# Performance work log

Hardware: AMD Instinct MI355X
Metric: run time of the kernel (lower is better)

Reference implementation:

```python
import jax, jax.numpy as jnp
import numpy as np

N, E, D, H = 20000, 320000, 128, 256
NUM_FINE = 2


def _mlp(x, W1, b1, W2, b2):
    # Linear -> relu -> Linear -> relu (dropout rate 0.0 is identity)
    h = jax.nn.relu(x @ W1 + b1)
    return jax.nn.relu(h @ W2 + b2)


def setup_inputs() -> dict:
    key = jax.random.key(0)
    ks = jax.random.split(key, 12)

    def p(k, shape):
        fan_in = shape[0]
        return jax.random.normal(k, shape, jnp.float32) * (1.0 / fan_in) ** 0.5

    return {
        "nodes": jax.random.normal(ks[0], (N, D), jnp.float32),
        "edges": jax.random.normal(ks[1], (E, D), jnp.float32),
        "senders": jax.random.randint(ks[2], (E,), 0, N, jnp.int32),
        "receivers": jax.random.randint(ks[3], (E,), 0, N, jnp.int32),
        # embed node MLP: D -> H -> D
        "Wn1": p(ks[4], (D, H)), "bn1": jnp.zeros((H,), jnp.float32),
        "Wn2": p(ks[5], (H, D)), "bn2": jnp.zeros((D,), jnp.float32),
        # embed edge MLP: D -> H -> D
        "We1": p(ks[6], (D, H)), "be1": jnp.zeros((H,), jnp.float32),
        "We2": p(ks[7], (H, D)), "be2": jnp.zeros((D,), jnp.float32),
        # edge model MLP: 3D -> H -> D  (concat[src, dest, edge_attr])
        "Wed1": p(ks[8], (3 * D, H)), "bed1": jnp.zeros((H,), jnp.float32),
        "Wed2": p(ks[9], (H, D)), "bed2": jnp.zeros((D,), jnp.float32),
        # node model MLP: 2D -> H -> D  (concat[x, segment_sum(edge_attr)])
        "Wnd1": p(ks[10], (2 * D, H)), "bnd1": jnp.zeros((H,), jnp.float32),
        "Wnd2": p(ks[11], (H, D)), "bnd2": jnp.zeros((D,), jnp.float32),
    }


def reference(nodes, edges, senders, receivers,
              Wn1, bn1, Wn2, bn2, We1, be1, We2, be2,
              Wed1, bed1, Wed2, bed2, Wnd1, bnd1, Wnd2, bnd2):
    # Embed stage (EmbedMetaLayer)
    x = _mlp(nodes, Wn1, bn1, Wn2, bn2)   # (N, D)
    e = _mlp(edges, We1, be1, We2, be2)   # (E, D)

    pooled = []
    for _ in range(NUM_FINE):
        # EdgeModel: gather src/dest node feats, concat with edge feats, MLP
        edge_in = jnp.concatenate([x[senders], x[receivers], e], axis=-1)  # (E, 3D)
        e = _mlp(edge_in, Wed1, bed1, Wed2, bed2)                           # (E, D)
        # NodeModel: scatter-add edge feats to receiver nodes, concat, MLP
        agg = jax.ops.segment_sum(e, receivers, num_segments=N)            # (N, D)
        x = _mlp(jnp.concatenate([x, agg], axis=-1), Wnd1, bnd1, Wnd2, bnd2)  # (N, D)
        # global_add_pooling: vmap(jnp.sum) over nodes -> per-node feature sum (N,)
        pooled.append(jnp.sum(x, axis=-1))
    # concatenate along last axis of the 1-D pooled vectors -> (NUM_FINE * N,)
    return jnp.concatenate(pooled, axis=-1)
```

## Files before the change

### kernel.cpp

```cpp
#include <hip/hip_runtime.h>
#include <stdint.h>

#define N_NODES 20000
#define N_EDGES 320000

typedef __attribute__((ext_vector_type(8)))  __bf16        bf16x8;
typedef __attribute__((ext_vector_type(16))) float         f32x16;
typedef __attribute__((ext_vector_type(4)))  float         f32x4v;
typedef __attribute__((ext_vector_type(4)))  uint32_t      u32x4;
typedef __attribute__((ext_vector_type(8)))  unsigned short us8;
typedef __attribute__((ext_vector_type(2)))  unsigned short us2;

static __device__ __forceinline__ unsigned short cvt_bf16(float f) {
  uint32_t u = __builtin_bit_cast(uint32_t, f);
  u = (u + 0x7fffu + ((u >> 16) & 1u)) >> 16;
  return (unsigned short)u;
}
static __device__ __forceinline__ float cvt_f32(unsigned short h) {
  uint32_t u = ((uint32_t)h) << 16;
  return __builtin_bit_cast(float, u);
}

static __device__ __forceinline__ void gll16(const void* g, void* l) {
  __builtin_amdgcn_global_load_lds(
      (const __attribute__((address_space(1))) unsigned int*)g,
      (__attribute__((address_space(3))) unsigned int*)l, 16, 0, 0);
}

__global__ void pack_w(const float* __restrict__ W, unsigned short* __restrict__ out,
                       int K, int Ncols) {
  int idx = blockIdx.x * 256 + threadIdx.x;
  int total = K * Ncols;
  if (idx >= total) return;
  int e    = idx & 7;
  int lane = (idx >> 3) & 63;
  int t    = idx >> 9;
  int ntiles = Ncols >> 5;
  int nt = t % ntiles;
  int ks = t / ntiles;
  int k = ks * 16 + (lane >> 5) * 8 + e;
  int c = nt * 32 + (lane & 31);
  out[idx] = cvt_bf16(W[(size_t)k * Ncols + c]);
}

__global__ void pack_w2(const float* __restrict__ W, unsigned short* __restrict__ out) {
  int idx = blockIdx.x * 256 + threadIdx.x;
  if (idx >= 32768) return;
  int e    = idx & 7;
  int lane = (idx >> 3) & 63;
  int t    = idx >> 9;
  int nt = t & 3, ks = t >> 2;
  int k = ks * 16 + ((lane >> 5) << 2) + (e & 3) + ((e >> 2) << 3);
  int c = nt * 32 + (lane & 31);
  out[idx] = cvt_bf16(W[(size_t)k * 128 + c]);
}

__global__ void hist_k(const int* __restrict__ recv, int* __restrict__ cnt, int n) {
  int i = blockIdx.x * 256 + threadIdx.x;
  if (i < n) atomicAdd(&cnt[recv[i]], 1);
}

__global__ void scan_k(const int* __restrict__ cnt, int* __restrict__ off,
                       int* __restrict__ cursor, int n) {
  __shared__ int part[1024];
  int t = threadIdx.x;
  int chunk = (n + 1023) / 1024;
  int base = t * chunk;
  int s = 0;
  for (int i = 0; i < chunk; ++i) { int idx = base + i; if (idx < n) s += cnt[idx]; }
  part[t] = s;
  __syncthreads();
  for (int d = 1; d < 1024; d <<= 1) {
    int v = (t >= d) ? part[t - d] : 0;
    __syncthreads();
    part[t] += v;
    __syncthreads();
  }
  int prefix = (t > 0) ? part[t - 1] : 0;
  for (int i = 0; i < chunk; ++i) {
    int idx = base + i;
    if (idx < n) { off[idx] = prefix; cursor[idx] = prefix; prefix += cnt[idx]; }
  }
  if (t == 1023) off[n] = part[1023];
}

__global__ void fill_k(const int* __restrict__ recv, int* __restrict__ cursor,
                       int* __restrict__ eid, int n) {
  int i = blockIdx.x * 256 + threadIdx.x;
  if (i < n) {
    int p = atomicAdd(&cursor[recv[i]], 1);
    eid[p] = i;
  }
}

__global__ void agg_k(const unsigned short* __restrict__ eb, const int* __restrict__ off,
                      const int* __restrict__ eid, unsigned short* __restrict__ aggb, int n) {
  int node = blockIdx.x * 4 + (threadIdx.x >> 6);
  if (node >= n) return;
  int lane = threadIdx.x & 63;
  float a0 = 0.f, a1 = 0.f;
  int s = off[node], t = off[node + 1];
  for (int q = s; q < t; ++q) {
    int ei = eid[q];
    us2 v = *(const us2*)(eb + (size_t)ei * 128 + lane * 2);
    a0 += cvt_f32(v[0]);
    a1 += cvt_f32(v[1]);
  }
  us2 r; r[0] = cvt_bf16(a0); r[1] = cvt_bf16(a1);
  *(us2*)(aggb + (size_t)node * 128 + lane * 2) = r;
}

template <int KIN, int MODE, int POOL>
__global__ __launch_bounds__(256, 2)
void mlp_kernel(const float* __restrict__ srcf,
                const unsigned short* __restrict__ xb,
                const unsigned short* __restrict__ ebuf,
                const unsigned short* __restrict__ aggb,
                const int* __restrict__ senders,
                const int* __restrict__ receivers,
                const unsigned short* __restrict__ P1,
                const float* __restrict__ b1,
                const unsigned short* __restrict__ P2,
                const float* __restrict__ b2,
                unsigned short* __restrict__ dst,
                float* __restrict__ pool_out,
                int nrows) {
  constexpr int NS1 = KIN / 32;
  __shared__ __align__(16) unsigned char lds[32768];

  const int tid  = threadIdx.x;
  const int lane = tid & 63;
  const int wid  = tid >> 6;
  const int g    = lane >> 5;
  const int l31  = lane & 31;
  const int rowBlock = blockIdx.x << 7;

  const unsigned char* P1b = (const unsigned char*)P1;
  const unsigned char* P2b = (const unsigned char*)P2;

  int grow = rowBlock + wid * 32 + l31;
  if (grow >= nrows) grow = nrows - 1;

  const unsigned short *pS = nullptr, *pR = nullptr, *pE = nullptr;
  const unsigned short *pX = nullptr, *pAg = nullptr;
  const float* fb = nullptr;
  if constexpr (MODE == 0) {
    fb = srcf + (size_t)grow * KIN;
  } else if constexpr (MODE == 1) {
    pS = xb + (size_t)senders[grow] * 128;
    pR = xb + (size_t)receivers[grow] * 128;
    pE = ebuf + (size_t)grow * 128;
  } else {
    pX  = xb + (size_t)grow * 128;
    pAg = aggb + (size_t)grow * 128;
  }

  auto STG1 = [&](int s) {
    unsigned char* bW = lds + (s & 1) * 16384;
#pragma unroll
    for (int c = 0; c < 4; ++c)
      gll16(P1b + (size_t)s * 16384 + c * 4096 + tid * 16,
            bW + c * 4096 + wid * 1024);
  };
  auto STG2 = [&](int c) {
    unsigned char* bW = lds + (c & 1) * 16384;
#pragma unroll
    for (int q = 0; q < 4; ++q)
      gll16(P2b + (size_t)c * 16384 + q * 4096 + tid * 16,
            bW + q * 4096 + wid * 1024);
  };

  auto LROW = [&](int s, us8& o0, us8& o1) {
    const int k0s = s * 32;
    const unsigned short* p;
    if constexpr (MODE == 1) {
      const int seg = k0s >> 7;
      p = (seg == 0) ? pS : (seg == 1) ? pR : pE;
    } else {
      p = (k0s >> 7) ? pAg : pX;
    }
    const int ko = k0s & 127;
    o0 = *(const us8*)(p + ko + g * 8);
    o1 = *(const us8*)(p + ko + 16 + g * 8);
  };
  auto LROWF = [&](int s, f32x4v* rf) {
    const float* p = fb + s * 32 + g * 8;
    rf[0] = *(const f32x4v*)(p);
    rf[1] = *(const f32x4v*)(p + 4);
    rf[2] = *(const f32x4v*)(p + 16);
    rf[3] = *(const f32x4v*)(p + 20);
  };
  auto MKBR = [&](const f32x4v* rf, bf16x8& b0v, bf16x8& b1v) {
    us8 h0, h1;
#pragma unroll
    for (int e = 0; e < 4; ++e) {
      h0[e] = cvt_bf16(rf[0][e]); h0[4 + e] = cvt_bf16(rf[1][e]);
      h1[e] = cvt_bf16(rf[2][e]); h1[4 + e] = cvt_bf16(rf[3][e]);
    }
    b0v = __builtin_bit_cast(bf16x8, h0);
    b1v = __builtin_bit_cast(bf16x8, h1);
  };

  f32x16 acc1[8];
#pragma unroll
  for (int t = 0; t < 8; ++t)
#pragma unroll
    for (int k = 0; k < 16; ++k) acc1[t][k] = 0.0f;

  auto COMPUTE = [&](const unsigned char* bW, bf16x8 b0v, bf16x8 b1v) {
    __builtin_amdgcn_s_setprio(1);
#pragma unroll
    for (int kc = 0; kc < 2; ++kc) {
      const bf16x8 bv = kc ? b1v : b0v;
#pragma unroll
      for (int nt = 0; nt < 8; ++nt) {
        bf16x8 av = __builtin_bit_cast(bf16x8,
            *(const us8*)(bW + (kc * 8 + nt) * 1024 + lane * 16));
        acc1[nt] = __builtin_amdgcn_mfma_f32_32x32x16_bf16(av, bv, acc1[nt], 0, 0, 0);
      }
    }
    __builtin_amdgcn_s_setprio(0);
  };

  constexpr int CNT = (MODE == 0) ? 8 : 6;

  us8 rA0, rA1, rB0, rB1;
  f32x4v rfA[4], rfB[4];

  STG1(0);
  if constexpr (MODE == 0) LROWF(0, rfA); else LROW(0, rA0, rA1);

#pragma unroll 1
  for (int s = 0; s < NS1; s += 2) {
    STG1(s + 1);
    if constexpr (MODE == 0) LROWF(s + 1, rfB); else LROW(s + 1, rB0, rB1);
    asm volatile("s_waitcnt vmcnt(%0)" :: "i"(CNT) : "memory");
    asm volatile("s_barrier" ::: "memory");
    {
      bf16x8 b0v, b1v;
      if constexpr (MODE == 0) MKBR(rfA, b0v, b1v);
      else { b0v = __builtin_bit_cast(bf16x8, rA0); b1v = __builtin_bit_cast(bf16x8, rA1); }
      COMPUTE(lds, b0v, b1v);
    }
    asm volatile("s_waitcnt lgkmcnt(0)" ::: "memory");
    asm volatile("s_barrier" ::: "memory");

    const bool more = (s + 2 < NS1);
    if (more) {
      STG1(s + 2);
      if constexpr (MODE == 0) LROWF(s + 2, rfA); else LROW(s + 2, rA0, rA1);
      asm volatile("s_waitcnt vmcnt(%0)" :: "i"(CNT) : "memory");
    } else {
      asm volatile("s_waitcnt vmcnt(0)" ::: "memory");
    }
    asm volatile("s_barrier" ::: "memory");
    {
      bf16x8 b0v, b1v;
      if constexpr (MODE == 0) MKBR(rfB, b0v, b1v);
      else { b0v = __builtin_bit_cast(bf16x8, rB0); b1v = __builtin_bit_cast(bf16x8, rB1); }
      COMPUTE(lds + 16384, b0v, b1v);
    }
    if (more) {
      asm volatile("s_waitcnt lgkmcnt(0)" ::: "memory");
      asm volatile("s_barrier" ::: "memory");
    }
  }

  f32x4v bb[8];
#pragma unroll
  for (int t = 0; t < 8; ++t)
    bb[t] = *(const f32x4v*)(b1 + t * 32 + (lane & 7) * 4);

  STG2(0);
  asm volatile("s_waitcnt lgkmcnt(0)" ::: "memory");
  asm volatile("s_barrier" ::: "memory");
  STG2(1);

  u32x4 pa4[16];
#pragma unroll
  for (int t = 0; t < 8; ++t) {
#pragma unroll
    for (int q4 = 0; q4 < 4; ++q4) {
      const f32x4v bv4 = *(const f32x4v*)(b1 + t * 32 + q4 * 8 + g * 4);
      float v0 = fmaxf(acc1[t][q4 * 4 + 0] + bv4[0], 0.0f);
      float v1 = fmaxf(acc1[t][q4 * 4 + 1] + bv4[1], 0.0f);
      float v2 = fmaxf(acc1[t][q4 * 4 + 2] + bv4[2], 0.0f);
      float v3 = fmaxf(acc1[t][q4 * 4 + 3] + bv4[3], 0.0f);
      uint32_t lo, hi;
      asm("v_cvt_pk_bf16_f32 %0, %1, %2" : "=v"(lo) : "v"(v0), "v"(v1));
      asm("v_cvt_pk_bf16_f32 %0, %1, %2" : "=v"(hi) : "v"(v2), "v"(v3));
      pa4[t * 2 + (q4 >> 1)][(q4 & 1) * 2 + 0] = lo;
      pa4[t * 2 + (q4 >> 1)][(q4 & 1) * 2 + 1] = hi;
    }
  }

  f32x16 acc2[4];
#pragma unroll
  for (int nt = 0; nt < 4; ++nt)
#pragma unroll
    for (int k = 0; k < 16; ++k) acc2[nt][k] = 0.0f;

#pragma unroll
  for (int c = 0; c < 4; ++c) {
    if (c < 3) asm volatile("s_waitcnt vmcnt(4)" ::: "memory");
    else       asm volatile("s_waitcnt vmcnt(0)" ::: "memory");
    asm volatile("s_barrier" ::: "memory");
    const unsigned char* bW = lds + (c & 1) * 16384;
    __builtin_amdgcn_s_setprio(1);
#pragma unroll
    for (int kk = 0; kk < 4; ++kk) {
      const bf16x8 a2 = __builtin_bit_cast(bf16x8, pa4[c * 4 + kk]);
#pragma unroll
      for (int nt = 0; nt < 4; ++nt) {
        const bf16x8 bw = __builtin_bit_cast(bf16x8,
            *(const us8*)(bW + (kk * 4 + nt) * 1024 + lane * 16));
        acc2[nt] = __builtin_amdgcn_mfma_f32_32x32x16_bf16(a2, bw, acc2[nt], 0, 0, 0);
      }
    }
    __builtin_amdgcn_s_setprio(0);
    asm volatile("s_waitcnt lgkmcnt(0)" ::: "memory");
    asm volatile("s_barrier" ::: "memory");
    if (c + 2 < 4) STG2(c + 2);
  }

  float bias2[4];
#pragma unroll
  for (int nt = 0; nt < 4; ++nt) bias2[nt] = b2[nt * 32 + l31];

#pragma unroll
  for (int reg = 0; reg < 16; ++reg) {
    const int rowpat = (reg & 3) + ((reg >> 2) << 3) + g * 4;
    const int row = rowBlock + wid * 32 + rowpat;
    float vs = 0.0f;
#pragma unroll
    for (int nt = 0; nt < 4; ++nt) {
      float v = fmaxf(acc2[nt][reg] + bias2[nt], 0.0f);
      vs += v;
      if (row < nrows) dst[(size_t)row * 128 + nt * 32 + l31] = cvt_bf16(v);
    }
    if constexpr (POOL) {
#pragma unroll
      for (int m = 1; m <= 16; m <<= 1) vs += __shfl_xor(vs, m, 64);
      if (l31 == 0 && row < nrows) pool_out[row] = vs;
    }
  }
}

static constexpr size_t OFF_X    = 0;
static constexpr size_t OFF_E    = 5120000;
static constexpr size_t OFF_AGG  = 87040000;
static constexpr size_t OFF_PN1  = 92160000;
static constexpr size_t OFF_PN2  = OFF_PN1 + 65536;
static constexpr size_t OFF_PE1  = OFF_PN2 + 65536;
static constexpr size_t OFF_PE2  = OFF_PE1 + 65536;
static constexpr size_t OFF_PD1  = OFF_PE2 + 65536;
static constexpr size_t OFF_PD2  = OFF_PD1 + 196608;
static constexpr size_t OFF_PM1  = OFF_PD2 + 65536;
static constexpr size_t OFF_PM2  = OFF_PM1 + 131072;
static constexpr size_t OFF_CNT  = OFF_PM2 + 65536;
static constexpr size_t OFF_OFFS = OFF_CNT + 80000;
static constexpr size_t OFF_CUR  = OFF_OFFS + 80004;
static constexpr size_t OFF_EID  = OFF_CUR + 80000;

extern "C" void kernel_launch(void* const* d_in, const int* in_sizes, int n_in,
                              void* d_out, int out_size, void* d_ws, size_t ws_size,
                              hipStream_t stream) {
  const float* nodes = (const float*)d_in[0];
  const float* edges = (const float*)d_in[1];
  const int* senders = (const int*)d_in[2];
  const int* receivers = (const int*)d_in[3];
  const float* Wn1 = (const float*)d_in[4];  const float* bn1 = (const float*)d_in[5];
  const float* Wn2 = (const float*)d_in[6];  const float* bn2 = (const float*)d_in[7];
  const float* We1 = (const float*)d_in[8];  const float* be1 = (const float*)d_in[9];
  const float* We2 = (const float*)d_in[10]; const float* be2 = (const float*)d_in[11];
  const float* Wed1 = (const float*)d_in[12]; const float* bed1 = (const float*)d_in[13];
  const float* Wed2 = (const float*)d_in[14]; const float* bed2 = (const float*)d_in[15];
  const float* Wnd1 = (const float*)d_in[16]; const float* bnd1 = (const float*)d_in[17];
  const float* Wnd2 = (const float*)d_in[18]; const float* bnd2 = (const float*)d_in[19];

  char* ws = (char*)d_ws;
  unsigned short* xb   = (unsigned short*)(ws + OFF_X);
  unsigned short* eb   = (unsigned short*)(ws + OFF_E);
  unsigned short* aggb = (unsigned short*)(ws + OFF_AGG);
  unsigned short* Pn1  = (unsigned short*)(ws + OFF_PN1);
  unsigned short* Pn2  = (unsigned short*)(ws + OFF_PN2);
  unsigned short* Pe1  = (unsigned short*)(ws + OFF_PE1);
  unsigned short* Pe2  = (unsigned short*)(ws + OFF_PE2);
  unsigned short* Pd1  = (unsigned short*)(ws + OFF_PD1);
  unsigned short* Pd2  = (unsigned short*)(ws + OFF_PD2);
  unsigned short* Pm1  = (unsigned short*)(ws + OFF_PM1);
  unsigned short* Pm2  = (unsigned short*)(ws + OFF_PM2);
  int* cnt    = (int*)(ws + OFF_CNT);
  int* offs   = (int*)(ws + OFF_OFFS);
  int* cursor = (int*)(ws + OFF_CUR);
  int* eid    = (int*)(ws + OFF_EID);
  float* outp = (float*)d_out;

  pack_w<<<128, 256, 0, stream>>>(Wn1, Pn1, 128, 256);
  pack_w2<<<128, 256, 0, stream>>>(Wn2, Pn2);
  pack_w<<<128, 256, 0, stream>>>(We1, Pe1, 128, 256);
  pack_w2<<<128, 256, 0, stream>>>(We2, Pe2);
  pack_w<<<384, 256, 0, stream>>>(Wed1, Pd1, 384, 256);
  pack_w2<<<128, 256, 0, stream>>>(Wed2, Pd2);
  pack_w<<<256, 256, 0, stream>>>(Wnd1, Pm1, 256, 256);
  pack_w2<<<128, 256, 0, stream>>>(Wnd2, Pm2);

  hipMemsetAsync(cnt, 0, (size_t)N_NODES * 4, stream);
  hist_k<<<1250, 256, 0, stream>>>(receivers, cnt, N_EDGES);
  scan_k<<<1, 1024, 0, stream>>>(cnt, offs, cursor, N_NODES);
  fill_k<<<1250, 256, 0, stream>>>(receivers, cursor, eid, N_EDGES);

  const int nodeBlocks = (N_NODES + 127) / 128;
  const int edgeBlocks = N_EDGES / 128;

  mlp_kernel<128, 0, 0><<<nodeBlocks, 256, 0, stream>>>(
      nodes, nullptr, nullptr, nullptr, nullptr, nullptr,
      Pn1, bn1, Pn2, bn2, xb, nullptr, N_NODES);
  mlp_kernel<128, 0, 0><<<edgeBlocks, 256, 0, stream>>>(
      edges, nullptr, nullptr, nullptr, nullptr, nullptr,
      Pe1, be1, Pe2, be2, eb, nullptr, N_EDGES);

  for (int it = 0; it < 2; ++it) {
    mlp_kernel<384, 1, 0><<<edgeBlocks, 256, 0, stream>>>(
        nullptr, xb, eb, nullptr, senders, receivers,
        Pd1, bed1, Pd2, bed2, eb, nullptr, N_EDGES);
    agg_k<<<(N_NODES + 3) / 4, 256, 0, stream>>>(eb, offs, eid, aggb, N_NODES);
    mlp_kernel<256, 2, 1><<<nodeBlocks, 256, 0, stream>>>(
        nullptr, xb, nullptr, aggb, nullptr, nullptr,
        Pm1, bnd1, Pm2, bnd2, xb, outp + (size_t)it * N_NODES, N_NODES);
  }
}
```

Measured before the change: 515.5 us.

## Triple-buffer weight staging in LDS and raise occupancy to three blocks

Moves the MLP kernel's weight staging from double to triple buffering in a 48KB LDS area, which cuts synchronisation to one barrier per K-step. The input-row register prefetch is deepened to three stages ahead and the loop is fully unrolled. Second-layer weight staging now starts right after each barrier instead of at the end of the step. Launch bounds are raised to three blocks per CU to hide more latency, at the cost of a tighter VGPR budget that may cause spills, and more LDS per block.

```diff
diff --git a/kernel.cpp b/kernel.cpp
--- a/kernel.cpp
+++ b/kernel.cpp
@@ -26,6 +26,14 @@
       (const __attribute__((address_space(1))) unsigned int*)g,
       (__attribute__((address_space(3))) unsigned int*)l, 16, 0, 0);
 }
+
+#define WAITV(n) do { \
+  if ((n) == 0)      asm volatile("s_waitcnt vmcnt(0)" ::: "memory"); \
+  else if ((n) == 2) asm volatile("s_waitcnt vmcnt(2)" ::: "memory"); \
+  else if ((n) == 4) asm volatile("s_waitcnt vmcnt(4)" ::: "memory"); \
+  else if ((n) == 6) asm volatile("s_waitcnt vmcnt(6)" ::: "memory"); \
+  else               asm volatile("s_waitcnt vmcnt(8)" ::: "memory"); \
+} while (0)
 
 __global__ void pack_w(const float* __restrict__ W, unsigned short* __restrict__ out,
                        int K, int Ncols) {
@@ -111,7 +119,7 @@
 }
 
 template <int KIN, int MODE, int POOL>
-__global__ __launch_bounds__(256, 2)
+__global__ __launch_bounds__(256, 3)
 void mlp_kernel(const float* __restrict__ srcf,
                 const unsigned short* __restrict__ xb,
                 const unsigned short* __restrict__ ebuf,
@@ -126,7 +134,8 @@
                 float* __restrict__ pool_out,
                 int nrows) {
   constexpr int NS1 = KIN / 32;
-  __shared__ __align__(16) unsigned char lds[32768];
+  constexpr int ROWOPS = (MODE == 0) ? 4 : 2;
+  __shared__ __align__(16) unsigned char lds[49152];
 
   const int tid  = threadIdx.x;
   const int lane = tid & 63;
@@ -156,21 +165,21 @@
   }
 
   auto STG1 = [&](int s) {
-    unsigned char* bW = lds + (s & 1) * 16384;
+    unsigned char* bW = lds + (s % 3) * 16384;
 #pragma unroll
     for (int c = 0; c < 4; ++c)
       gll16(P1b + (size_t)s * 16384 + c * 4096 + tid * 16,
             bW + c * 4096 + wid * 1024);
   };
   auto STG2 = [&](int c) {
-    unsigned char* bW = lds + (c & 1) * 16384;
+    unsigned char* bW = lds + ((c + NS1) % 3) * 16384;
 #pragma unroll
     for (int q = 0; q < 4; ++q)
       gll16(P2b + (size_t)c * 16384 + q * 4096 + tid * 16,
             bW + q * 4096 + wid * 1024);
   };
 
-  auto LROW = [&](int s, us8& o0, us8& o1) {
+  auto LROW = [&](int s, us8* o) {
     const int k0s = s * 32;
     const unsigned short* p;
     if constexpr (MODE == 1) {
@@ -180,8 +189,8 @@
       p = (k0s >> 7) ? pAg : pX;
     }
     const int ko = k0s & 127;
-    o0 = *(const us8*)(p + ko + g * 8);
-    o1 = *(const us8*)(p + ko + 16 + g * 8);
+    o[0] = *(const us8*)(p + ko + g * 8);
+    o[1] = *(const us8*)(p + ko + 16 + g * 8);
   };
   auto LROWF = [&](int s, f32x4v* rf) {
     const float* p = fb + s * 32 + g * 8;
@@ -222,58 +231,32 @@
     __builtin_amdgcn_s_setprio(0);
   };
 
-  constexpr int CNT = (MODE == 0) ? 8 : 6;
-
-  us8 rA0, rA1, rB0, rB1;
-  f32x4v rfA[4], rfB[4];
+  us8    rr[4][2];
+  f32x4v rf[4][4];
 
   STG1(0);
-  if constexpr (MODE == 0) LROWF(0, rfA); else LROW(0, rA0, rA1);
-
-#pragma unroll 1
-  for (int s = 0; s < NS1; s += 2) {
-    STG1(s + 1);
-    if constexpr (MODE == 0) LROWF(s + 1, rfB); else LROW(s + 1, rB0, rB1);
-    asm volatile("s_waitcnt vmcnt(%0)" :: "i"(CNT) : "memory");
-    asm volatile("s_barrier" ::: "memory");
-    {
-      bf16x8 b0v, b1v;
-      if constexpr (MODE == 0) MKBR(rfA, b0v, b1v);
-      else { b0v = __builtin_bit_cast(bf16x8, rA0); b1v = __builtin_bit_cast(bf16x8, rA1); }
-      COMPUTE(lds, b0v, b1v);
-    }
+  if constexpr (MODE == 0) { LROWF(0, rf[0]); LROWF(1, rf[1]); LROWF(2, rf[2]); }
+  else                     { LROW(0, rr[0]);  LROW(1, rr[1]);  LROW(2, rr[2]); }
+
+#pragma unroll
+  for (int s = 0; s < NS1; ++s) {
+    const int w = (s == 0) ? ROWOPS * 2 : ((s + 2 < NS1) ? ROWOPS : 0);
+    WAITV(w);
     asm volatile("s_waitcnt lgkmcnt(0)" ::: "memory");
     asm volatile("s_barrier" ::: "memory");
-
-    const bool more = (s + 2 < NS1);
-    if (more) {
-      STG1(s + 2);
-      if constexpr (MODE == 0) LROWF(s + 2, rfA); else LROW(s + 2, rA0, rA1);
-      asm volatile("s_waitcnt vmcnt(%0)" :: "i"(CNT) : "memory");
-    } else {
-      asm volatile("s_waitcnt vmcnt(0)" ::: "memory");
-    }
-    asm volatile("s_barrier" ::: "memory");
-    {
-      bf16x8 b0v, b1v;
-      if constexpr (MODE == 0) MKBR(rfB, b0v, b1v);
-      else { b0v = __builtin_bit_cast(bf16x8, rB0); b1v = __builtin_bit_cast(bf16x8, rB1); }
-      COMPUTE(lds + 16384, b0v, b1v);
-    }
-    if (more) {
-      asm volatile("s_waitcnt lgkmcnt(0)" ::: "memory");
-      asm volatile("s_barrier" ::: "memory");
-    }
-  }
-
-  f32x4v bb[8];
-#pragma unroll
-  for (int t = 0; t < 8; ++t)
-    bb[t] = *(const f32x4v*)(b1 + t * 32 + (lane & 7) * 4);
+    if (s + 1 < NS1) STG1(s + 1);
+    if (s + 3 < NS1) {
+      if constexpr (MODE == 0) LROWF(s + 3, rf[(s + 3) & 3]);
+      else                     LROW(s + 3, rr[(s + 3) & 3]);
+    }
+    bf16x8 b0v, b1v;
+    if constexpr (MODE == 0) MKBR(rf[s & 3], b0v, b1v);
+    else { b0v = __builtin_bit_cast(bf16x8, rr[s & 3][0]);
+           b1v = __builtin_bit_cast(bf16x8, rr[s & 3][1]); }
+    COMPUTE(lds + (s % 3) * 16384, b0v, b1v);
+  }
 
   STG2(0);
-  asm volatile("s_waitcnt lgkmcnt(0)" ::: "memory");
-  asm volatile("s_barrier" ::: "memory");
   STG2(1);
 
   u32x4 pa4[16];
@@ -302,10 +285,11 @@
 
 #pragma unroll
   for (int c = 0; c < 4; ++c) {
-    if (c < 3) asm volatile("s_waitcnt vmcnt(4)" ::: "memory");
-    else       asm volatile("s_waitcnt vmcnt(0)" ::: "memory");
+    WAITV(c < 3 ? 4 : 0);
+    asm volatile("s_waitcnt lgkmcnt(0)" ::: "memory");
     asm volatile("s_barrier" ::: "memory");
-    const unsigned char* bW = lds + (c & 1) * 16384;
+    if (c + 2 < 4) STG2(c + 2);
+    const unsigned char* bW = lds + ((c + NS1) % 3) * 16384;
     __builtin_amdgcn_s_setprio(1);
 #pragma unroll
     for (int kk = 0; kk < 4; ++kk) {
@@ -318,9 +302,6 @@
       }
     }
     __builtin_amdgcn_s_setprio(0);
-    asm volatile("s_waitcnt lgkmcnt(0)" ::: "memory");
-    asm volatile("s_barrier" ::: "memory");
-    if (c + 2 < 4) STG2(c + 2);
   }
 
   float bias2[4];
```

After: 944.0 us. +83.1%, slower.
